# Kernel optimization log

Measured on AMD Instinct MI355X. Metric: run time of the kernel, lower is better.

The kernel has to match this reference:

```python
import jax, jax.numpy as jnp
import numpy as np

WS = 8          # window size M
SHIFT = WS // 2 # cyclic shift
HEADS = 8


def _rel_pos_index(ws):
    # (ws*ws, ws*ws) indices into the (2ws-1)^2 bias table
    coords = np.stack(np.meshgrid(np.arange(ws), np.arange(ws), indexing='ij'), 0).reshape(2, -1)
    rel = coords[:, :, None] - coords[:, None, :]          # (2, N, N)
    rel = rel.transpose(1, 2, 0) + (ws - 1)                # shift to [0, 2ws-2]
    return rel[..., 0] * (2 * ws - 1) + rel[..., 1]        # (N, N)


def _shift_mask(H, W, ws, shift):
    # standard Swin attention mask for shifted windows: (nWin, N, N)
    img = np.zeros((H, W), dtype=np.int32)
    cnt = 0
    for hs in (slice(0, -ws), slice(-ws, -shift), slice(-shift, None)):
        for wsl in (slice(0, -ws), slice(-ws, -shift), slice(-shift, None)):
            img[hs, wsl] = cnt
            cnt += 1
    mw = img.reshape(H // ws, ws, W // ws, ws).transpose(0, 2, 1, 3).reshape(-1, ws * ws)
    diff = mw[:, None, :] - mw[:, :, None]
    return np.where(diff != 0, -100.0, 0.0).astype(np.float32)


def setup_inputs() -> dict:
    key = jax.random.key(0)
    ks = jax.random.split(key, 6)
    B, C, H, W = 32, 256, 64, 64
    return {
        'x': jax.random.normal(ks[0], (B, C, H, W), jnp.float32),
        'w_qkv': jax.random.normal(ks[1], (C, 3 * C), jnp.float32) * (C ** -0.5),
        'b_qkv': jnp.zeros((3 * C,), jnp.float32),
        'w_o': jax.random.normal(ks[2], (C, C), jnp.float32) * (C ** -0.5),
        'b_o': jnp.zeros((C,), jnp.float32),
        'rel_bias_table': jax.random.normal(ks[3], ((2 * WS - 1) ** 2, HEADS), jnp.float32) * 0.02,
    }


def reference(x, w_qkv, b_qkv, w_o, b_o, rel_bias_table):
    B, C, H, W = x.shape
    ws, shift, heads = WS, SHIFT, HEADS
    dh = C // heads
    nH, nW = H // ws, W // ws
    nWin, N = nH * nW, ws * ws

    rel_idx = jnp.asarray(_rel_pos_index(ws))                 # (N, N) int
    mask = jnp.asarray(_shift_mask(H, W, ws, shift))          # (nWin, N, N)

    # cyclic shift
    xs = jnp.roll(x, (-shift, -shift), axis=(2, 3))
    # window partition: (B, C, H, W) -> (B, nWin, N, C)
    xw = xs.reshape(B, C, nH, ws, nW, ws).transpose(0, 2, 4, 3, 5, 1).reshape(B, nWin, N, C)

    qkv = xw @ w_qkv + b_qkv                                  # (B, nWin, N, 3C)
    qkv = qkv.reshape(B, nWin, N, 3, heads, dh)
    q = qkv[..., 0, :, :].transpose(0, 1, 3, 2, 4)            # (B, nWin, h, N, dh)
    k = qkv[..., 1, :, :].transpose(0, 1, 3, 2, 4)
    v = qkv[..., 2, :, :].transpose(0, 1, 3, 2, 4)

    attn = jnp.einsum('bwhnd,bwhmd->bwhnm', q, k) * (dh ** -0.5)
    bias = rel_bias_table[rel_idx]                            # (N, N, heads)
    attn = attn + bias.transpose(2, 0, 1)[None, None]         # add rel pos bias
    attn = attn + mask[None, :, None]                         # add shift mask
    attn = jax.nn.softmax(attn, axis=-1)

    out = jnp.einsum('bwhnm,bwhmd->bwhnd', attn, v)           # (B, nWin, h, N, dh)
    out = out.transpose(0, 1, 3, 2, 4).reshape(B, nWin, N, C)
    out = out @ w_o + b_o

    # window reverse: (B, nWin, N, C) -> (B, C, H, W)
    out = out.reshape(B, nH, nW, ws, ws, C).transpose(0, 5, 1, 3, 2, 4).reshape(B, C, H, W)
    # reverse cyclic shift
    return jnp.roll(out, (shift, shift), axis=(2, 3))
```

## Files before the change

kernel.cpp:

```cpp
#include <hip/hip_runtime.h>
#include <stdint.h>

typedef __attribute__((ext_vector_type(8))) short short8;
typedef __attribute__((ext_vector_type(4))) float floatx4;
typedef unsigned short u16;
typedef unsigned int u32;

#define MFMA16(a,b,c) __builtin_amdgcn_mfma_f32_16x16x32_bf16((a),(b),(c),0,0,0)

__device__ __forceinline__ u16 f2b(float f){
  u32 i; __builtin_memcpy(&i,&f,4); i += 0x7FFFu + ((i>>16)&1u); return (u16)(i>>16);
}
__device__ __forceinline__ int regid(int p){ return (p<56)?0:((p<60)?1:2); }

#define SCO 16896
#define LDS_ELEMS 26112

__global__ void prep_w(const float* __restrict__ wqkv, const float* __restrict__ wo,
                       u16* __restrict__ wqkvT, u16* __restrict__ woT){
  int idx = blockIdx.x*256 + threadIdx.x;
  if(idx < 768*256){ int n = idx>>8, k = idx&255; wqkvT[idx] = f2b(wqkv[k*768 + n]); }
  else { int j = idx - 768*256; int n = j>>8, k = j&255; woT[j] = f2b(wo[k*256 + n]); }
}

__global__ __launch_bounds__(256,3) void swmsa_attn(
    const float* __restrict__ x, const u16* __restrict__ wqkvT, const float* __restrict__ bqkv,
    const float* __restrict__ table, u16* __restrict__ yws)
{
  extern __shared__ u16 lds[];
  const int tid  = threadIdx.x;
  const int wave = tid>>6, lane = tid&63;
  const int quad = lane>>4, colid = lane&15;
  const int bi = blockIdx.x;
  const int xcd = bi & 7, j = bi >> 3;
  const int r0 = ((j >> 3) << 3) | xcd;
  const int wx = j & 7;
  const int b = r0 >> 3, wy = r0 & 7;
  const size_t imgbase = (size_t)b*256*4096;
  const int w0 = wx*8+4;
  const floatx4 fzero = {0.f,0.f,0.f,0.f};
  u16* sc = lds + SCO + wave*2304;

  for(int i=0;i<2;++i){
    int unit = tid + 256*i;
    int cg = unit>>3, ty = unit&7;
    int hs = (wy*8+ty+4)&63;
    u16 vv[4][8];
    #pragma unroll
    for(int cc=0;cc<4;++cc){
      const float* src = x + imgbase + (size_t)(cg*4+cc)*4096 + (size_t)hs*64;
      floatx4 lo, hi;
      if(wx<7){ lo = *(const floatx4*)(src+w0); hi = *(const floatx4*)(src+w0+4); }
      else    { lo = *(const floatx4*)(src+60); hi = *(const floatx4*)(src); }
      #pragma unroll
      for(int t=0;t<4;++t){ vv[cc][t]=f2b(lo[t]); vv[cc][4+t]=f2b(hi[t]); }
    }
    #pragma unroll
    for(int t=0;t<8;++t){
      uint64_t pk = (uint64_t)vv[0][t] | ((uint64_t)vv[1][t]<<16)
                  | ((uint64_t)vv[2][t]<<32) | ((uint64_t)vv[3][t]<<48);
      *(uint64_t*)&lds[(ty*8+t)*264 + cg*4] = pk;
    }
  }
  __syncthreads();

  short8 aq2[2][4], bk2[2][4], bv2[2][2][2];
  for(int t3=0; t3<3; ++t3){
    const int cc = 2 - t3;
    const int col0 = (cc*4 + wave)*64;
    const u16* wslab = wqkvT + (size_t)(col0+colid)*256 + quad*8;
    floatx4 acc[4][4];
    #pragma unroll
    for(int mt=0;mt<4;++mt)
      #pragma unroll
      for(int nt=0;nt<4;++nt) acc[mt][nt] = fzero;
    short8 bcur[4], bnxt[4];
    #pragma unroll
    for(int nt=0;nt<4;++nt) bcur[nt] = *(const short8*)&wslab[(size_t)nt*16*256];
    for(int k0=0;k0<256;k0+=32){
      short8 af[4];
      #pragma unroll
      for(int mt=0;mt<4;++mt) af[mt]  = *(const short8*)&lds[(mt*16+colid)*264 + k0 + quad*8];
      if(k0 < 224){
        #pragma unroll
        for(int nt=0;nt<4;++nt) bnxt[nt] = *(const short8*)&wslab[(size_t)nt*16*256 + k0 + 32];
      }
      #pragma unroll
      for(int mt=0;mt<4;++mt)
        #pragma unroll
        for(int nt=0;nt<4;++nt) acc[mt][nt] = MFMA16(af[mt], bcur[nt], acc[mt][nt]);
      #pragma unroll
      for(int nt=0;nt<4;++nt) bcur[nt] = bnxt[nt];
    }
    #pragma unroll
    for(int hf=0; hf<2; ++hf){
      #pragma unroll
      for(int nt2=0; nt2<2; ++nt2){
        int nt = hf*2 + nt2;
        float bias = bqkv[col0 + nt*16 + colid];
        #pragma unroll
        for(int mt=0;mt<4;++mt)
          #pragma unroll
          for(int rr=0;rr<4;++rr){
            int row = mt*16 + quad*4 + rr;
            u16 bvv = f2b(acc[mt][nt][rr] + bias);
            if(cc==2) sc[(nt2*16+colid)*72 + row] = bvv;
            else      sc[row*36 + nt2*16 + colid] = bvv;
          }
      }
      if(cc==2){
        #pragma unroll
        for(int n2=0;n2<2;++n2)
          #pragma unroll
          for(int kc=0;kc<2;++kc)
            bv2[hf][n2][kc] = *(const short8*)&sc[(n2*16+colid)*72 + kc*32 + quad*8];
      } else if(cc==1){
        #pragma unroll
        for(int mt=0;mt<4;++mt) bk2[hf][mt] = *(const short8*)&sc[(mt*16+colid)*36 + quad*8];
      } else {
        #pragma unroll
        for(int mt=0;mt<4;++mt) aq2[hf][mt] = *(const short8*)&sc[(mt*16+colid)*36 + quad*8];
      }
    }
  }
  __syncthreads();

  const float scale = 0.17677669529663687f;
  #pragma unroll
  for(int hi=0; hi<2; ++hi){
    const int h = wave*2 + hi;
    floatx4 s[4][4];
    #pragma unroll
    for(int mt=0;mt<4;++mt)
      #pragma unroll
      for(int nt=0;nt<4;++nt) s[mt][nt] = MFMA16(aq2[hi][mt], bk2[hi][nt], fzero);
    int cntk[4], kys[4], kxs[4];
    #pragma unroll
    for(int nt=0;nt<4;++nt){
      int col = nt*16 + colid;
      kys[nt] = col>>3; kxs[nt] = col&7;
      cntk[nt] = regid(wy*8 + kys[nt])*3 + regid(wx*8 + kxs[nt]);
    }
    #pragma unroll
    for(int mt=0;mt<4;++mt)
      #pragma unroll
      for(int rr=0;rr<4;++rr){
        int row = mt*16 + quad*4 + rr;
        int ty = row>>3, tx = row&7;
        int cntq = regid(wy*8+ty)*3 + regid(wx*8+tx);
        #pragma unroll
        for(int nt=0;nt<4;++nt){
          int rel = (ty - kys[nt] + 7)*15 + (tx - kxs[nt] + 7);
          float add = table[rel*8 + h] + ((cntq==cntk[nt]) ? 0.f : -100.f);
          s[mt][nt][rr] = s[mt][nt][rr]*scale + add;
        }
      }
    u32 gpk[4][4];
    #pragma unroll
    for(int mt=0;mt<4;++mt)
      #pragma unroll
      for(int rr=0;rr<4;++rr){
        float mx = s[mt][0][rr];
        #pragma unroll
        for(int nt=1;nt<4;++nt) mx = fmaxf(mx, s[mt][nt][rr]);
        #pragma unroll
        for(int d=1; d<16; d<<=1) mx = fmaxf(mx, __shfl_xor(mx, d));
        float e[4], sum = 0.f;
        #pragma unroll
        for(int nt=0;nt<4;++nt){ e[nt] = __expf(s[mt][nt][rr]-mx); sum += e[nt]; }
        #pragma unroll
        for(int d=1; d<16; d<<=1) sum += __shfl_xor(sum, d);
        float inv = 1.0f/sum;
        int row = mt*16 + quad*4 + rr;
        sc[row*36 + colid]      = f2b(e[0]*inv);
        sc[row*36 + 16 + colid] = f2b(e[1]*inv);
        gpk[mt][rr] = (u32)f2b(e[2]*inv) | ((u32)f2b(e[3]*inv) << 16);
      }
    floatx4 o[4][2];
    #pragma unroll
    for(int mt=0;mt<4;++mt){ o[mt][0]=fzero; o[mt][1]=fzero; }
    #pragma unroll
    for(int kc=0;kc<2;++kc){
      if(kc==1){
        #pragma unroll
        for(int mt=0;mt<4;++mt)
          #pragma unroll
          for(int rr=0;rr<4;++rr){
            int row = mt*16 + quad*4 + rr;
            sc[row*36 + colid]      = (u16)(gpk[mt][rr] & 0xffffu);
            sc[row*36 + 16 + colid] = (u16)(gpk[mt][rr] >> 16);
          }
      }
      short8 ap[4];
      #pragma unroll
      for(int mt=0;mt<4;++mt) ap[mt] = *(const short8*)&sc[(mt*16+colid)*36 + quad*8];
      #pragma unroll
      for(int mt=0;mt<4;++mt)
        #pragma unroll
        for(int n2=0;n2<2;++n2) o[mt][n2] = MFMA16(ap[mt], bv2[hi][n2][kc], o[mt][n2]);
    }
    #pragma unroll
    for(int n2=0;n2<2;++n2){
      int c = h*32 + n2*16 + colid;
      #pragma unroll
      for(int mt=0;mt<4;++mt)
        #pragma unroll
        for(int rr=0;rr<4;++rr)
          lds[(mt*16+quad*4+rr)*264 + c] = f2b(o[mt][n2][rr]);
    }
  }
  __syncthreads();

  const size_t bandbase = (size_t)r0 * (512*256);
  #pragma unroll
  for(int i=0;i<8;++i){
    int unit = i*256 + tid;
    int tokw = unit>>5, c8 = unit&31;
    int tyw = tokw>>3, txw = tokw&7;
    int cg = (8*wx + 4 + txw) & 63;
    size_t t = (size_t)(tyw*64 + cg);
    *(short8*)&yws[bandbase + t*256 + c8*8] = *(const short8*)&lds[tokw*264 + c8*8];
  }
}

__global__ __launch_bounds__(256,3) void swmsa_proj(
    const u16* __restrict__ yws, const u16* __restrict__ woT,
    const float* __restrict__ bo, float* __restrict__ out)
{
  __shared__ u16 tile[2][256*32];
  const int tid = threadIdx.x;
  const int wave = tid>>6, lane = tid&63;
  const int quad = lane>>4, colid = lane&15;
  const int bi = blockIdx.x;
  const int x7 = bi&7, jj = bi>>3;
  const int band = ((jj>>3)<<3) | x7;
  const int sub = jj&7, h2 = sub>>2, npp = sub&3;
  const int b = band>>3, wy = band&7;
  const u16* ybase = yws + (size_t)band*(512*256) + (size_t)h2*(256*256);
  const int ch = npp*64 + wave*16 + colid;
  const u16* wbase = woT + (size_t)ch*256 + quad*8;
  const floatx4 fzero = {0.f,0.f,0.f,0.f};
  floatx4 acc[16];
  #pragma unroll
  for(int mt=0;mt<16;++mt) acc[mt]=fzero;

  const int rbase0 = tid>>2, slot = tid&3;
  const int swz = (tid>>3)&3;
  const int rsw = (colid>>1)&3;

  short8 sv[4];
  #pragma unroll
  for(int i=0;i<4;++i)
    sv[i] = *(const short8*)&ybase[(size_t)(i*64 + rbase0)*256 + slot*8];
  #pragma unroll
  for(int i=0;i<4;++i)
    *(short8*)&tile[0][(i*64+rbase0)*32 + ((slot^swz))*8] = sv[i];
  __syncthreads();

  for(int kk=0;kk<8;++kk){
    const int cur = kk&1;
    if(kk<7){
      #pragma unroll
      for(int i=0;i<4;++i)
        sv[i] = *(const short8*)&ybase[(size_t)(i*64 + rbase0)*256 + (kk+1)*32 + slot*8];
    }
    short8 bw = *(const short8*)&wbase[kk*32];
    #pragma unroll
    for(int mt=0;mt<16;++mt){
      short8 a = *(const short8*)&tile[cur][(mt*16+colid)*32 + ((quad^rsw))*8];
      acc[mt] = MFMA16(a, bw, acc[mt]);
    }
    if(kk<7){
      #pragma unroll
      for(int i=0;i<4;++i)
        *(short8*)&tile[cur^1][(i*64+rbase0)*32 + ((slot^swz))*8] = sv[i];
    }
    __syncthreads();
  }

  const float bias = bo[ch];
  float* obase = out + (size_t)b*256*4096 + (size_t)ch*4096;
  #pragma unroll
  for(int mt=0;mt<16;++mt){
    int ty = mt>>2;
    int hd = (wy*8 + h2*4 + ty + 4) & 63;
    int colb = (mt&3)*16 + quad*4;
    floatx4 v = acc[mt];
    v[0]+=bias; v[1]+=bias; v[2]+=bias; v[3]+=bias;
    *(floatx4*)(obase + (size_t)hd*64 + colb) = v;
  }
}

__global__ __launch_bounds__(256,3) void swmsa_fused(
    const float* __restrict__ x, const u16* __restrict__ wqkvT, const float* __restrict__ bqkv,
    const u16* __restrict__ woT, const float* __restrict__ bo, const float* __restrict__ table,
    float* __restrict__ out)
{
  extern __shared__ u16 lds[];
  const int tid  = threadIdx.x;
  const int wave = tid>>6, lane = tid&63;
  const int quad = lane>>4, colid = lane&15;
  const int bi = blockIdx.x;
  const int xcd = bi & 7, j = bi >> 3;
  const int r0 = ((j >> 3) << 3) | xcd;
  const int wx = j & 7;
  const int b = r0 >> 3, wy = r0 & 7;
  const size_t imgbase = (size_t)b*256*4096;
  const int w0 = wx*8+4;
  const floatx4 fzero = {0.f,0.f,0.f,0.f};
  u16* sc = lds + SCO + wave*2304;

  for(int i=0;i<2;++i){
    int unit = tid + 256*i;
    int cg = unit>>3, ty = unit&7;
    int hs = (wy*8+ty+4)&63;
    u16 vv[4][8];
    #pragma unroll
    for(int cc=0;cc<4;++cc){
      const float* src = x + imgbase + (size_t)(cg*4+cc)*4096 + (size_t)hs*64;
      floatx4 lo, hi;
      if(wx<7){ lo = *(const floatx4*)(src+w0); hi = *(const floatx4*)(src+w0+4); }
      else    { lo = *(const floatx4*)(src+60); hi = *(const floatx4*)(src); }
      #pragma unroll
      for(int t=0;t<4;++t){ vv[cc][t]=f2b(lo[t]); vv[cc][4+t]=f2b(hi[t]); }
    }
    #pragma unroll
    for(int t=0;t<8;++t){
      uint64_t pk = (uint64_t)vv[0][t] | ((uint64_t)vv[1][t]<<16)
                  | ((uint64_t)vv[2][t]<<32) | ((uint64_t)vv[3][t]<<48);
      *(uint64_t*)&lds[(ty*8+t)*264 + cg*4] = pk;
    }
  }
  __syncthreads();

  short8 aq2[2][4], bk2[2][4], bv2[2][2][2];
  for(int t3=0; t3<3; ++t3){
    const int cc = 2 - t3;
    const int col0 = (cc*4 + wave)*64;
    const u16* wslab = wqkvT + (size_t)(col0+colid)*256 + quad*8;
    floatx4 acc[4][4];
    #pragma unroll
    for(int mt=0;mt<4;++mt)
      #pragma unroll
      for(int nt=0;nt<4;++nt) acc[mt][nt] = fzero;
    short8 bcur[4], bnxt[4];
    #pragma unroll
    for(int nt=0;nt<4;++nt) bcur[nt] = *(const short8*)&wslab[(size_t)nt*16*256];
    for(int k0=0;k0<256;k0+=32){
      short8 af[4];
      #pragma unroll
      for(int mt=0;mt<4;++mt) af[mt]  = *(const short8*)&lds[(mt*16+colid)*264 + k0 + quad*8];
      if(k0 < 224){
        #pragma unroll
        for(int nt=0;nt<4;++nt) bnxt[nt] = *(const short8*)&wslab[(size_t)nt*16*256 + k0 + 32];
      }
      #pragma unroll
      for(int mt=0;mt<4;++mt)
        #pragma unroll
        for(int nt=0;nt<4;++nt) acc[mt][nt] = MFMA16(af[mt], bcur[nt], acc[mt][nt]);
      #pragma unroll
      for(int nt=0;nt<4;++nt) bcur[nt] = bnxt[nt];
    }
    #pragma unroll
    for(int hf=0; hf<2; ++hf){
      #pragma unroll
      for(int nt2=0; nt2<2; ++nt2){
        int nt = hf*2 + nt2;
        float bias = bqkv[col0 + nt*16 + colid];
        #pragma unroll
        for(int mt=0;mt<4;++mt)
          #pragma unroll
          for(int rr=0;rr<4;++rr){
            int row = mt*16 + quad*4 + rr;
            u16 bvv = f2b(acc[mt][nt][rr] + bias);
            if(cc==2) sc[(nt2*16+colid)*72 + row] = bvv;
            else      sc[row*36 + nt2*16 + colid] = bvv;
          }
      }
      if(cc==2){
        #pragma unroll
        for(int n2=0;n2<2;++n2)
          #pragma unroll
          for(int kc=0;kc<2;++kc)
            bv2[hf][n2][kc] = *(const short8*)&sc[(n2*16+colid)*72 + kc*32 + quad*8];
      } else if(cc==1){
        #pragma unroll
        for(int mt=0;mt<4;++mt) bk2[hf][mt] = *(const short8*)&sc[(mt*16+colid)*36 + quad*8];
      } else {
        #pragma unroll
        for(int mt=0;mt<4;++mt) aq2[hf][mt] = *(const short8*)&sc[(mt*16+colid)*36 + quad*8];
      }
    }
  }
  __syncthreads();

  const float scale = 0.17677669529663687f;
  #pragma unroll
  for(int hi=0; hi<2; ++hi){
    const int h = wave*2 + hi;
    floatx4 s[4][4];
    #pragma unroll
    for(int mt=0;mt<4;++mt)
      #pragma unroll
      for(int nt=0;nt<4;++nt) s[mt][nt] = MFMA16(aq2[hi][mt], bk2[hi][nt], fzero);
    int cntk[4], kys[4], kxs[4];
    #pragma unroll
    for(int nt=0;nt<4;++nt){
      int col = nt*16 + colid;
      kys[nt] = col>>3; kxs[nt] = col&7;
      cntk[nt] = regid(wy*8 + kys[nt])*3 + regid(wx*8 + kxs[nt]);
    }
    #pragma unroll
    for(int mt=0;mt<4;++mt)
      #pragma unroll
      for(int rr=0;rr<4;++rr){
        int row = mt*16 + quad*4 + rr;
        int ty = row>>3, tx = row&7;
        int cntq = regid(wy*8+ty)*3 + regid(wx*8+tx);
        #pragma unroll
        for(int nt=0;nt<4;++nt){
          int rel = (ty - kys[nt] + 7)*15 + (tx - kxs[nt] + 7);
          float add = table[rel*8 + h] + ((cntq==cntk[nt]) ? 0.f : -100.f);
          s[mt][nt][rr] = s[mt][nt][rr]*scale + add;
        }
      }
    u32 gpk[4][4];
    #pragma unroll
    for(int mt=0;mt<4;++mt)
      #pragma unroll
      for(int rr=0;rr<4;++rr){
        float mx = s[mt][0][rr];
        #pragma unroll
        for(int nt=1;nt<4;++nt) mx = fmaxf(mx, s[mt][nt][rr]);
        #pragma unroll
        for(int d=1; d<16; d<<=1) mx = fmaxf(mx, __shfl_xor(mx, d));
        float e[4], sum = 0.f;
        #pragma unroll
        for(int nt=0;nt<4;++nt){ e[nt] = __expf(s[mt][nt][rr]-mx); sum += e[nt]; }
        #pragma unroll
        for(int d=1; d<16; d<<=1) sum += __shfl_xor(sum, d);
        float inv = 1.0f/sum;
        int row = mt*16 + quad*4 + rr;
        sc[row*36 + colid]      = f2b(e[0]*inv);
        sc[row*36 + 16 + colid] = f2b(e[1]*inv);
        gpk[mt][rr] = (u32)f2b(e[2]*inv) | ((u32)f2b(e[3]*inv) << 16);
      }
    floatx4 o[4][2];
    #pragma unroll
    for(int mt=0;mt<4;++mt){ o[mt][0]=fzero; o[mt][1]=fzero; }
    #pragma unroll
    for(int kc=0;kc<2;++kc){
      if(kc==1){
        #pragma unroll
        for(int mt=0;mt<4;++mt)
          #pragma unroll
          for(int rr=0;rr<4;++rr){
            int row = mt*16 + quad*4 + rr;
            sc[row*36 + colid]      = (u16)(gpk[mt][rr] & 0xffffu);
            sc[row*36 + 16 + colid] = (u16)(gpk[mt][rr] >> 16);
          }
      }
      short8 ap[4];
      #pragma unroll
      for(int mt=0;mt<4;++mt) ap[mt] = *(const short8*)&sc[(mt*16+colid)*36 + quad*8];
      #pragma unroll
      for(int mt=0;mt<4;++mt)
        #pragma unroll
        for(int n2=0;n2<2;++n2) o[mt][n2] = MFMA16(ap[mt], bv2[hi][n2][kc], o[mt][n2]);
    }
    #pragma unroll
    for(int n2=0;n2<2;++n2){
      int c = h*32 + n2*16 + colid;
      #pragma unroll
      for(int mt=0;mt<4;++mt)
        #pragma unroll
        for(int rr=0;rr<4;++rr)
          lds[(mt*16+quad*4+rr)*264 + c] = f2b(o[mt][n2][rr]);
    }
  }
  __syncthreads();

  {
    floatx4 acc[4][4];
    #pragma unroll
    for(int np=0;np<4;++np)
      #pragma unroll
      for(int mt=0;mt<4;++mt) acc[np][mt] = fzero;
    const u16* wbase = woT + (size_t)(wave*16+colid)*256 + quad*8;
    for(int k0=0;k0<256;k0+=32){
      short8 ay[4];
      #pragma unroll
      for(int mt=0;mt<4;++mt) ay[mt] = *(const short8*)&lds[(mt*16+colid)*264 + k0 + quad*8];
      #pragma unroll
      for(int np=0;np<4;++np){
        short8 bw = *(const short8*)&wbase[(size_t)np*16384 + k0];
        #pragma unroll
        for(int mt=0;mt<4;++mt) acc[np][mt] = MFMA16(ay[mt], bw, acc[np][mt]);
      }
    }
    const int ty_base = quad>>1, txg = quad&1;
    const int col = (wx<7) ? (w0 + 4*txg) : (txg ? 0 : 60);
    #pragma unroll
    for(int np=0;np<4;++np){
      const int ch = np*64 + wave*16 + colid;
      const float bias = bo[ch];
      float* chbase = out + imgbase + (size_t)ch*4096;
      #pragma unroll
      for(int mt=0;mt<4;++mt){
        int ty = 2*mt + ty_base;
        int hd = (wy*8 + ty + 4)&63;
        floatx4 vsto = acc[np][mt];
        vsto[0]+=bias; vsto[1]+=bias; vsto[2]+=bias; vsto[3]+=bias;
        *(floatx4*)(chbase + (size_t)hd*64 + col) = vsto;
      }
    }
  }
}

extern "C" void kernel_launch(void* const* d_in, const int* in_sizes, int n_in,
                              void* d_out, int out_size, void* d_ws, size_t ws_size,
                              hipStream_t stream) {
  const float* x     = (const float*)d_in[0];
  const float* wqkv  = (const float*)d_in[1];
  const float* bqkv  = (const float*)d_in[2];
  const float* wo    = (const float*)d_in[3];
  const float* bo    = (const float*)d_in[4];
  const float* table = (const float*)d_in[5];
  float* out = (float*)d_out;

  u16* wqkvT = (u16*)d_ws;
  u16* woT   = wqkvT + 768*256;
  u16* yws   = woT   + 256*256;

  const size_t need = (size_t)(768*256 + 256*256)*2 + (size_t)256*512*256*2;

  prep_w<<<1024, 256, 0, stream>>>(wqkv, wo, wqkvT, woT);

  if(ws_size >= need){
    (void)hipFuncSetAttribute((const void*)swmsa_attn,
                              hipFuncAttributeMaxDynamicSharedMemorySize, LDS_ELEMS*2);
    swmsa_attn<<<2048, 256, LDS_ELEMS*2, stream>>>(x, wqkvT, bqkv, table, yws);
    swmsa_proj<<<2048, 256, 0, stream>>>(yws, woT, bo, out);
  } else {
    (void)hipFuncSetAttribute((const void*)swmsa_fused,
                              hipFuncAttributeMaxDynamicSharedMemorySize, LDS_ELEMS*2);
    swmsa_fused<<<2048, 256, LDS_ELEMS*2, stream>>>(x, wqkvT, bqkv, woT, bo, table, out);
  }
}
```

Before: 473.6 us.

## Keep QKV and softmax fragments in registers via lane shuffles instead of LDS scratch

Restructures the attention kernel so each head's Q/K/V projection is computed with a transposed MFMA layout (S^T = K·Q^T), and the bf16 fragments are redistributed between lanes with __shfl instead of round-tripping through per-wave LDS scratch. This drops the LDS scratch region (ATTN_ELEMS instead of 26112 elements), which may allow more resident blocks, and folds the softmax scale into Q. It also raises the proj kernel's launch-bounds occupancy hint. The cost is more shuffle instructions, the loss of the old weight-prefetch double buffering, and possibly higher register pressure from computing heads one at a time.

```diff
diff --git a/kernel.cpp b/kernel.cpp
--- a/kernel.cpp
+++ b/kernel.cpp
@@ -11,16 +11,171 @@
 __device__ __forceinline__ u16 f2b(float f){
   u32 i; __builtin_memcpy(&i,&f,4); i += 0x7FFFu + ((i>>16)&1u); return (u16)(i>>16);
 }
+__device__ __forceinline__ u32 pk2(float a, float b){
+  return (u32)f2b(a) | ((u32)f2b(b)<<16);
+}
 __device__ __forceinline__ int regid(int p){ return (p<56)?0:((p<60)?1:2); }
 
+__device__ __forceinline__ short8 fragsel(const u32* pkA, const u32* pkB, int L0, int L1, bool hiq){
+  union { u32 w[4]; short8 s; } u;
+  u32 a, b;
+  a = (u32)__shfl((int)pkA[0], L0); b = (u32)__shfl((int)pkB[0], L0); u.w[0] = hiq ? b : a;
+  a = (u32)__shfl((int)pkA[1], L0); b = (u32)__shfl((int)pkB[1], L0); u.w[1] = hiq ? b : a;
+  a = (u32)__shfl((int)pkA[0], L1); b = (u32)__shfl((int)pkB[0], L1); u.w[2] = hiq ? b : a;
+  a = (u32)__shfl((int)pkA[1], L1); b = (u32)__shfl((int)pkB[1], L1); u.w[3] = hiq ? b : a;
+  return u.s;
+}
+
+#define ATTN_ELEMS 16896
 #define SCO 16896
-#define LDS_ELEMS 26112
+#define FUSED_ELEMS 26112
 
 __global__ void prep_w(const float* __restrict__ wqkv, const float* __restrict__ wo,
                        u16* __restrict__ wqkvT, u16* __restrict__ woT){
   int idx = blockIdx.x*256 + threadIdx.x;
   if(idx < 768*256){ int n = idx>>8, k = idx&255; wqkvT[idx] = f2b(wqkv[k*768 + n]); }
   else { int j = idx - 768*256; int n = j>>8, k = j&255; woT[j] = f2b(wo[k*256 + n]); }
+}
+
+__device__ __forceinline__ void run_head(
+    const u16* lds, const u16* __restrict__ wT, const float* __restrict__ bqkv,
+    const float* __restrict__ table, int wave, int hi, int colid, int quad,
+    int wy, int wx, u32 opk[2][4][2])
+{
+  const floatx4 fz = {0.f,0.f,0.f,0.f};
+  const int h = wave*2 + hi;
+  const int L0 = ((quad&1)<<5) + colid, L1 = L0 + 16;
+  const bool hiq = quad >= 2;
+  const float scale = 0.17677669529663687f;
+
+  u32 pkq[2][4][2], pkk[2][4][2];
+  #pragma unroll
+  for(int cc=0; cc<2; ++cc){
+    const int ch0 = (cc*4 + wave)*64 + hi*32;
+    const float sc = (cc==0) ? scale : 1.0f;
+    floatx4 acc[2][4];
+    #pragma unroll
+    for(int mt=0;mt<2;++mt)
+      #pragma unroll
+      for(int nt=0;nt<4;++nt) acc[mt][nt] = fz;
+    const u16* wbase = wT + (size_t)(ch0+colid)*256 + quad*8;
+    for(int k0=0;k0<256;k0+=32){
+      short8 xf[4], wf[2];
+      #pragma unroll
+      for(int nt=0;nt<4;++nt) xf[nt] = *(const short8*)&lds[(nt*16+colid)*264 + k0 + quad*8];
+      #pragma unroll
+      for(int mt=0;mt<2;++mt) wf[mt] = *(const short8*)&wbase[(size_t)mt*16*256 + k0];
+      #pragma unroll
+      for(int mt=0;mt<2;++mt)
+        #pragma unroll
+        for(int nt=0;nt<4;++nt) acc[mt][nt] = MFMA16(wf[mt], xf[nt], acc[mt][nt]);
+    }
+    #pragma unroll
+    for(int mt=0;mt<2;++mt){
+      floatx4 bb = *(const floatx4*)&bqkv[ch0 + mt*16 + quad*4];
+      #pragma unroll
+      for(int nt=0;nt<4;++nt){
+        u32 w0 = pk2((acc[mt][nt][0]+bb[0])*sc, (acc[mt][nt][1]+bb[1])*sc);
+        u32 w1 = pk2((acc[mt][nt][2]+bb[2])*sc, (acc[mt][nt][3]+bb[3])*sc);
+        if(cc==0){ pkq[mt][nt][0]=w0; pkq[mt][nt][1]=w1; }
+        else     { pkk[mt][nt][0]=w0; pkk[mt][nt][1]=w1; }
+      }
+    }
+  }
+  short8 qfr[4], kfr[4];
+  #pragma unroll
+  for(int T=0;T<4;++T){
+    qfr[T] = fragsel(pkq[0][T], pkq[1][T], L0, L1, hiq);
+    kfr[T] = fragsel(pkk[0][T], pkk[1][T], L0, L1, hiq);
+  }
+
+  short8 vfr[2][2];
+  {
+    const int chv = (8 + wave)*64 + hi*32;
+    floatx4 acc[4][2];
+    #pragma unroll
+    for(int mt=0;mt<4;++mt)
+      #pragma unroll
+      for(int nt=0;nt<2;++nt) acc[mt][nt] = fz;
+    const u16* wbase = wT + (size_t)(chv+colid)*256 + quad*8;
+    for(int k0=0;k0<256;k0+=32){
+      short8 xf[4], wf[2];
+      #pragma unroll
+      for(int mt=0;mt<4;++mt) xf[mt] = *(const short8*)&lds[(mt*16+colid)*264 + k0 + quad*8];
+      #pragma unroll
+      for(int nt=0;nt<2;++nt) wf[nt] = *(const short8*)&wbase[(size_t)nt*16*256 + k0];
+      #pragma unroll
+      for(int mt=0;mt<4;++mt)
+        #pragma unroll
+        for(int nt=0;nt<2;++nt) acc[mt][nt] = MFMA16(xf[mt], wf[nt], acc[mt][nt]);
+    }
+    u32 pkv[4][2][2];
+    #pragma unroll
+    for(int nt=0;nt<2;++nt){
+      float bv = bqkv[chv + nt*16 + colid];
+      #pragma unroll
+      for(int mt=0;mt<4;++mt){
+        pkv[mt][nt][0] = pk2(acc[mt][nt][0]+bv, acc[mt][nt][1]+bv);
+        pkv[mt][nt][1] = pk2(acc[mt][nt][2]+bv, acc[mt][nt][3]+bv);
+      }
+    }
+    #pragma unroll
+    for(int m=0;m<2;++m)
+      #pragma unroll
+      for(int kc=0;kc<2;++kc)
+        vfr[m][kc] = fragsel(pkv[2*kc][m], pkv[2*kc+1][m], L0, L1, hiq);
+  }
+
+  const int tqx = colid & 7;
+  const int rqx = regid(wx*8 + tqx);
+  #pragma unroll
+  for(int nq=0;nq<4;++nq){
+    const int tqy = 2*nq + (colid>>3);
+    const int cq = regid(wy*8 + tqy)*3 + rqx;
+    floatx4 s4[4];
+    #pragma unroll
+    for(int mt=0;mt<4;++mt) s4[mt] = MFMA16(kfr[mt], qfr[nq], fz);
+    #pragma unroll
+    for(int mt=0;mt<4;++mt){
+      const int tky = 2*mt + (quad>>1);
+      const int ry = (tqy - tky + 7)*15;
+      const int rk = regid(wy*8 + tky)*3;
+      #pragma unroll
+      for(int rr=0;rr<4;++rr){
+        const int tkx = (quad&1)*4 + rr;
+        const int ck = rk + regid(wx*8 + tkx);
+        const int rel = ry + (tqx - tkx + 7);
+        s4[mt][rr] += table[rel*8 + h] + ((cq==ck) ? 0.f : -100.f);
+      }
+    }
+    float mx = s4[0][0];
+    #pragma unroll
+    for(int mt=0;mt<4;++mt)
+      #pragma unroll
+      for(int rr=0;rr<4;++rr) mx = fmaxf(mx, s4[mt][rr]);
+    mx = fmaxf(mx, __shfl_xor(mx, 16));
+    mx = fmaxf(mx, __shfl_xor(mx, 32));
+    float sum = 0.f;
+    #pragma unroll
+    for(int mt=0;mt<4;++mt)
+      #pragma unroll
+      for(int rr=0;rr<4;++rr){ s4[mt][rr] = __expf(s4[mt][rr]-mx); sum += s4[mt][rr]; }
+    sum += __shfl_xor(sum, 16);
+    sum += __shfl_xor(sum, 32);
+    const float inv = 1.0f/sum;
+    u32 pkp[4][2];
+    #pragma unroll
+    for(int mt=0;mt<4;++mt){
+      pkp[mt][0] = pk2(s4[mt][0]*inv, s4[mt][1]*inv);
+      pkp[mt][1] = pk2(s4[mt][2]*inv, s4[mt][3]*inv);
+    }
+    short8 pf0 = fragsel(pkp[0], pkp[1], L0, L1, hiq);
+    short8 pf1 = fragsel(pkp[2], pkp[3], L0, L1, hiq);
+    floatx4 o0 = MFMA16(vfr[0][0], pf0, fz); o0 = MFMA16(vfr[0][1], pf1, o0);
+    floatx4 o1 = MFMA16(vfr[1][0], pf0, fz); o1 = MFMA16(vfr[1][1], pf1, o1);
+    opk[0][nq][0] = pk2(o0[0], o0[1]); opk[0][nq][1] = pk2(o0[2], o0[3]);
+    opk[1][nq][0] = pk2(o1[0], o1[1]); opk[1][nq][1] = pk2(o1[2], o1[3]);
+  }
 }
 
 __global__ __launch_bounds__(256,3) void swmsa_attn(
@@ -38,8 +193,6 @@
   const int b = r0 >> 3, wy = r0 & 7;
   const size_t imgbase = (size_t)b*256*4096;
   const int w0 = wx*8+4;
-  const floatx4 fzero = {0.f,0.f,0.f,0.f};
-  u16* sc = lds + SCO + wave*2304;
 
   for(int i=0;i<2;++i){
     int unit = tid + 256*i;
@@ -64,150 +217,23 @@
   }
   __syncthreads();
 
-  short8 aq2[2][4], bk2[2][4], bv2[2][2][2];
-  for(int t3=0; t3<3; ++t3){
-    const int cc = 2 - t3;
-    const int col0 = (cc*4 + wave)*64;
-    const u16* wslab = wqkvT + (size_t)(col0+colid)*256 + quad*8;
-    floatx4 acc[4][4];
-    #pragma unroll
-    for(int mt=0;mt<4;++mt)
-      #pragma unroll
-      for(int nt=0;nt<4;++nt) acc[mt][nt] = fzero;
-    short8 bcur[4], bnxt[4];
-    #pragma unroll
-    for(int nt=0;nt<4;++nt) bcur[nt] = *(const short8*)&wslab[(size_t)nt*16*256];
-    for(int k0=0;k0<256;k0+=32){
-      short8 af[4];
-      #pragma unroll
-      for(int mt=0;mt<4;++mt) af[mt]  = *(const short8*)&lds[(mt*16+colid)*264 + k0 + quad*8];
-      if(k0 < 224){
-        #pragma unroll
-        for(int nt=0;nt<4;++nt) bnxt[nt] = *(const short8*)&wslab[(size_t)nt*16*256 + k0 + 32];
-      }
-      #pragma unroll
-      for(int mt=0;mt<4;++mt)
-        #pragma unroll
-        for(int nt=0;nt<4;++nt) acc[mt][nt] = MFMA16(af[mt], bcur[nt], acc[mt][nt]);
-      #pragma unroll
-      for(int nt=0;nt<4;++nt) bcur[nt] = bnxt[nt];
-    }
-    #pragma unroll
-    for(int hf=0; hf<2; ++hf){
-      #pragma unroll
-      for(int nt2=0; nt2<2; ++nt2){
-        int nt = hf*2 + nt2;
-        float bias = bqkv[col0 + nt*16 + colid];
-        #pragma unroll
-        for(int mt=0;mt<4;++mt)
-          #pragma unroll
-          for(int rr=0;rr<4;++rr){
-            int row = mt*16 + quad*4 + rr;
-            u16 bvv = f2b(acc[mt][nt][rr] + bias);
-            if(cc==2) sc[(nt2*16+colid)*72 + row] = bvv;
-            else      sc[row*36 + nt2*16 + colid] = bvv;
-          }
-      }
-      if(cc==2){
-        #pragma unroll
-        for(int n2=0;n2<2;++n2)
-          #pragma unroll
-          for(int kc=0;kc<2;++kc)
-            bv2[hf][n2][kc] = *(const short8*)&sc[(n2*16+colid)*72 + kc*32 + quad*8];
-      } else if(cc==1){
-        #pragma unroll
-        for(int mt=0;mt<4;++mt) bk2[hf][mt] = *(const short8*)&sc[(mt*16+colid)*36 + quad*8];
-      } else {
-        #pragma unroll
-        for(int mt=0;mt<4;++mt) aq2[hf][mt] = *(const short8*)&sc[(mt*16+colid)*36 + quad*8];
-      }
-    }
-  }
-  __syncthreads();
-
-  const float scale = 0.17677669529663687f;
-  #pragma unroll
-  for(int hi=0; hi<2; ++hi){
-    const int h = wave*2 + hi;
-    floatx4 s[4][4];
-    #pragma unroll
-    for(int mt=0;mt<4;++mt)
-      #pragma unroll
-      for(int nt=0;nt<4;++nt) s[mt][nt] = MFMA16(aq2[hi][mt], bk2[hi][nt], fzero);
-    int cntk[4], kys[4], kxs[4];
-    #pragma unroll
-    for(int nt=0;nt<4;++nt){
-      int col = nt*16 + colid;
-      kys[nt] = col>>3; kxs[nt] = col&7;
-      cntk[nt] = regid(wy*8 + kys[nt])*3 + regid(wx*8 + kxs[nt]);
-    }
-    #pragma unroll
-    for(int mt=0;mt<4;++mt)
-      #pragma unroll
-      for(int rr=0;rr<4;++rr){
-        int row = mt*16 + quad*4 + rr;
-        int ty = row>>3, tx = row&7;
-        int cntq = regid(wy*8+ty)*3 + regid(wx*8+tx);
-        #pragma unroll
-        for(int nt=0;nt<4;++nt){
-          int rel = (ty - kys[nt] + 7)*15 + (tx - kxs[nt] + 7);
-          float add = table[rel*8 + h] + ((cntq==cntk[nt]) ? 0.f : -100.f);
-          s[mt][nt][rr] = s[mt][nt][rr]*scale + add;
+  u32 opk0[2][4][2], opk1[2][4][2];
+  run_head(lds, wqkvT, bqkv, table, wave, 0, colid, quad, wy, wx, opk0);
+  run_head(lds, wqkvT, bqkv, table, wave, 1, colid, quad, wy, wx, opk1);
+  __syncthreads();
+
+  #pragma unroll
+  for(int hi=0;hi<2;++hi){
+    #pragma unroll
+    for(int m=0;m<2;++m)
+      #pragma unroll
+      for(int nq=0;nq<4;++nq)
+        #pragma unroll
+        for(int p=0;p<2;++p){
+          int row = nq*16 + colid;
+          int ch = wave*64 + hi*32 + m*16 + quad*4 + p*2;
+          *(u32*)&lds[row*264 + ch] = hi ? opk1[m][nq][p] : opk0[m][nq][p];
         }
-      }
-    u32 gpk[4][4];
-    #pragma unroll
-    for(int mt=0;mt<4;++mt)
-      #pragma unroll
-      for(int rr=0;rr<4;++rr){
-        float mx = s[mt][0][rr];
-        #pragma unroll
-        for(int nt=1;nt<4;++nt) mx = fmaxf(mx, s[mt][nt][rr]);
-        #pragma unroll
-        for(int d=1; d<16; d<<=1) mx = fmaxf(mx, __shfl_xor(mx, d));
-        float e[4], sum = 0.f;
-        #pragma unroll
-        for(int nt=0;nt<4;++nt){ e[nt] = __expf(s[mt][nt][rr]-mx); sum += e[nt]; }
-        #pragma unroll
-        for(int d=1; d<16; d<<=1) sum += __shfl_xor(sum, d);
-        float inv = 1.0f/sum;
-        int row = mt*16 + quad*4 + rr;
-        sc[row*36 + colid]      = f2b(e[0]*inv);
-        sc[row*36 + 16 + colid] = f2b(e[1]*inv);
-        gpk[mt][rr] = (u32)f2b(e[2]*inv) | ((u32)f2b(e[3]*inv) << 16);
-      }
-    floatx4 o[4][2];
-    #pragma unroll
-    for(int mt=0;mt<4;++mt){ o[mt][0]=fzero; o[mt][1]=fzero; }
-    #pragma unroll
-    for(int kc=0;kc<2;++kc){
-      if(kc==1){
-        #pragma unroll
-        for(int mt=0;mt<4;++mt)
-          #pragma unroll
-          for(int rr=0;rr<4;++rr){
-            int row = mt*16 + quad*4 + rr;
-            sc[row*36 + colid]      = (u16)(gpk[mt][rr] & 0xffffu);
-            sc[row*36 + 16 + colid] = (u16)(gpk[mt][rr] >> 16);
-          }
-      }
-      short8 ap[4];
-      #pragma unroll
-      for(int mt=0;mt<4;++mt) ap[mt] = *(const short8*)&sc[(mt*16+colid)*36 + quad*8];
-      #pragma unroll
-      for(int mt=0;mt<4;++mt)
-        #pragma unroll
-        for(int n2=0;n2<2;++n2) o[mt][n2] = MFMA16(ap[mt], bv2[hi][n2][kc], o[mt][n2]);
-    }
-    #pragma unroll
-    for(int n2=0;n2<2;++n2){
-      int c = h*32 + n2*16 + colid;
-      #pragma unroll
-      for(int mt=0;mt<4;++mt)
-        #pragma unroll
-        for(int rr=0;rr<4;++rr)
-          lds[(mt*16+quad*4+rr)*264 + c] = f2b(o[mt][n2][rr]);
-    }
   }
   __syncthreads();
 
@@ -223,7 +249,7 @@
   }
 }
 
-__global__ __launch_bounds__(256,3) void swmsa_proj(
+__global__ __launch_bounds__(256,4) void swmsa_proj(
     const u16* __restrict__ yws, const u16* __restrict__ woT,
     const float* __restrict__ bo, float* __restrict__ out)
 {
@@ -537,13 +563,11 @@
   prep_w<<<1024, 256, 0, stream>>>(wqkv, wo, wqkvT, woT);
 
   if(ws_size >= need){
-    (void)hipFuncSetAttribute((const void*)swmsa_attn,
-                              hipFuncAttributeMaxDynamicSharedMemorySize, LDS_ELEMS*2);
-    swmsa_attn<<<2048, 256, LDS_ELEMS*2, stream>>>(x, wqkvT, bqkv, table, yws);
+    swmsa_attn<<<2048, 256, ATTN_ELEMS*2, stream>>>(x, wqkvT, bqkv, table, yws);
     swmsa_proj<<<2048, 256, 0, stream>>>(yws, woT, bo, out);
   } else {
     (void)hipFuncSetAttribute((const void*)swmsa_fused,
-                              hipFuncAttributeMaxDynamicSharedMemorySize, LDS_ELEMS*2);
-    swmsa_fused<<<2048, 256, LDS_ELEMS*2, stream>>>(x, wqkvT, bqkv, woT, bo, table, out);
-  }
-}
+                              hipFuncAttributeMaxDynamicSharedMemorySize, FUSED_ELEMS*2);
+    swmsa_fused<<<2048, 256, FUSED_ELEMS*2, stream>>>(x, wqkvT, bqkv, woT, bo, table, out);
+  }
+}
```

Result: slower. 649.7 us (+37.2%).

## Drop LDS staging in output projection, read A directly from global with smaller tiles

Applied to the files above, without the earlier changes.

The projection kernel no longer stages the attention output through a double-buffered LDS tile with barriers. Each wave now loads its A fragments straight from global memory. The block tile shrinks from 256 to 128 tokens and the grid doubles to 4096 blocks, with launch bounds relaxed to 2. This removes LDS traffic and syncs and adds parallelism, at the cost of redundant global/L2 reads of A across the four waves, which all read the same rows.

```diff
diff --git a/kernel.cpp b/kernel.cpp
--- a/kernel.cpp
+++ b/kernel.cpp
@@ -223,67 +223,43 @@
   }
 }
 
-__global__ __launch_bounds__(256,3) void swmsa_proj(
+__global__ __launch_bounds__(256,2) void swmsa_proj(
     const u16* __restrict__ yws, const u16* __restrict__ woT,
     const float* __restrict__ bo, float* __restrict__ out)
 {
-  __shared__ u16 tile[2][256*32];
   const int tid = threadIdx.x;
   const int wave = tid>>6, lane = tid&63;
   const int quad = lane>>4, colid = lane&15;
   const int bi = blockIdx.x;
-  const int x7 = bi&7, jj = bi>>3;
-  const int band = ((jj>>3)<<3) | x7;
-  const int sub = jj&7, h2 = sub>>2, npp = sub&3;
+  const int xcd = bi&7, jj = bi>>3;
+  const int band = ((jj>>4)<<3) | xcd;
+  const int sub = jj&15, q4 = sub>>2, npp = sub&3;
   const int b = band>>3, wy = band&7;
-  const u16* ybase = yws + (size_t)band*(512*256) + (size_t)h2*(256*256);
+  const u16* ybase = yws + (size_t)band*(512*256) + (size_t)q4*(128*256);
   const int ch = npp*64 + wave*16 + colid;
   const u16* wbase = woT + (size_t)ch*256 + quad*8;
-  const floatx4 fzero = {0.f,0.f,0.f,0.f};
-  floatx4 acc[16];
+  const u16* abase = ybase + (size_t)colid*256 + quad*8;
+  const floatx4 fz = {0.f,0.f,0.f,0.f};
+  floatx4 acc[8];
   #pragma unroll
-  for(int mt=0;mt<16;++mt) acc[mt]=fzero;
-
-  const int rbase0 = tid>>2, slot = tid&3;
-  const int swz = (tid>>3)&3;
-  const int rsw = (colid>>1)&3;
-
-  short8 sv[4];
+  for(int mt=0;mt<8;++mt) acc[mt]=fz;
+
   #pragma unroll
-  for(int i=0;i<4;++i)
-    sv[i] = *(const short8*)&ybase[(size_t)(i*64 + rbase0)*256 + slot*8];
-  #pragma unroll
-  for(int i=0;i<4;++i)
-    *(short8*)&tile[0][(i*64+rbase0)*32 + ((slot^swz))*8] = sv[i];
-  __syncthreads();
-
   for(int kk=0;kk<8;++kk){
-    const int cur = kk&1;
-    if(kk<7){
-      #pragma unroll
-      for(int i=0;i<4;++i)
-        sv[i] = *(const short8*)&ybase[(size_t)(i*64 + rbase0)*256 + (kk+1)*32 + slot*8];
-    }
     short8 bw = *(const short8*)&wbase[kk*32];
     #pragma unroll
-    for(int mt=0;mt<16;++mt){
-      short8 a = *(const short8*)&tile[cur][(mt*16+colid)*32 + ((quad^rsw))*8];
+    for(int mt=0;mt<8;++mt){
+      short8 a = *(const short8*)&abase[(size_t)mt*16*256 + kk*32];
       acc[mt] = MFMA16(a, bw, acc[mt]);
     }
-    if(kk<7){
-      #pragma unroll
-      for(int i=0;i<4;++i)
-        *(short8*)&tile[cur^1][(i*64+rbase0)*32 + ((slot^swz))*8] = sv[i];
-    }
-    __syncthreads();
   }
 
   const float bias = bo[ch];
   float* obase = out + (size_t)b*256*4096 + (size_t)ch*4096;
   #pragma unroll
-  for(int mt=0;mt<16;++mt){
+  for(int mt=0;mt<8;++mt){
     int ty = mt>>2;
-    int hd = (wy*8 + h2*4 + ty + 4) & 63;
+    int hd = (wy*8 + q4*2 + ty + 4) & 63;
     int colb = (mt&3)*16 + quad*4;
     floatx4 v = acc[mt];
     v[0]+=bias; v[1]+=bias; v[2]+=bias; v[3]+=bias;
@@ -540,7 +516,7 @@
     (void)hipFuncSetAttribute((const void*)swmsa_attn,
                               hipFuncAttributeMaxDynamicSharedMemorySize, LDS_ELEMS*2);
     swmsa_attn<<<2048, 256, LDS_ELEMS*2, stream>>>(x, wqkvT, bqkv, table, yws);
-    swmsa_proj<<<2048, 256, 0, stream>>>(yws, woT, bo, out);
+    swmsa_proj<<<4096, 256, 0, stream>>>(yws, woT, bo, out);
   } else {
     (void)hipFuncSetAttribute((const void*)swmsa_fused,
                               hipFuncAttributeMaxDynamicSharedMemorySize, LDS_ELEMS*2);
```

Result: slower. 559.3 us (+18.1%).
